# Performance work log

Measured on AMD Instinct MI355X. Metric: run time of the kernel, lower is better.

The kernel has to match this reference:

```python
import jax, jax.numpy as jnp
import numpy as np

T = 8            # num edge basis features (static)
E = 8388608      # num edges
N = 262144       # num output nodes
F = 64           # filters


def setup_inputs() -> dict:
    key = jax.random.key(0)
    k1, k2, k3 = jax.random.split(key, 3)
    edge_features = jax.random.normal(k1, (T, E), dtype=jnp.float32)
    sparse_indices = jax.random.randint(k2, (E, 2), 0, N, dtype=jnp.int64)
    kernel = jax.random.normal(k3, (T, F), dtype=jnp.float32) * 0.1
    bias = jnp.zeros((F,), dtype=jnp.float32)
    return {
        "edge_features": edge_features,
        "sparse_indices": sparse_indices,
        "out_size": N,
        "kernel": kernel,
        "bias": bias,
    }


def reference(edge_features, sparse_indices, out_size, kernel, bias):
    # edge_features: [T, E]; sparse_indices: [E, 2] (row = output node id)
    rows = sparse_indices[:, 0]
    # Aggregate per-edge features into nodes: [N, T]
    agg = jax.ops.segment_sum(edge_features.T, rows, num_segments=out_size)
    # Dense projection + bias (activation is None / linear)
    out = agg @ kernel + bias  # [N, F]
    return out
```

## Files before the change

kernel.cpp:

```cpp
#include <hip/hip_runtime.h>
#include <hip/hip_fp16.h>

typedef unsigned int uint;

#define T_DIM 8
#define F_DIM 64
#define BUCKETS 256
#define RPB 1024
#define RPB_SHIFT 10
#define CAP 36864
#define SC_BLOCKS 1024
#define SC_THREADS 512
#define SUB 2048
#define EPT (SUB / SC_THREADS)
#define NSUB 4
#define ACH 3072

__device__ __forceinline__ uint pack_h2(float a, float b) {
  union { __half2 h2; uint u32; } cvt;
  cvt.h2 = __floats2half2_rn(a, b);
  return cvt.u32;
}
__device__ __forceinline__ float2 unpack_h2(uint v) {
  union { uint u32; __half2 h2; } cvt;
  cvt.u32 = v;
  return __half22float2(cvt.h2);
}


__global__ __launch_bounds__(SC_THREADS) void scatter_sort_kernel(
    const uint* __restrict__ idx, const float* __restrict__ ef,
    uint* __restrict__ cursor, unsigned short* __restrict__ rows_out,
    uint4* __restrict__ recs_out, int E) {
  __shared__ uint hist[BUCKETS];
  __shared__ uint lbase[BUCKETS];
  __shared__ uint gdelta[BUCKETS];
  __shared__ uint wpart4[4];
  __shared__ uint wpre4[4];
  __shared__ uint srows[SUB];
  __shared__ uint4 srecs[SUB];
  __shared__ int s_is64;
  const int tid = threadIdx.x;
  const int lane = tid & 63;
  const int wid = tid >> 6;
  if (tid == 0) {
    uint acc = 0;
    for (int i = 1; i < 64; i += 2) acc |= idx[i];
    s_is64 = (acc == 0);
  }
  __syncthreads();
  const bool is64 = (s_is64 != 0);
  const int cstart = blockIdx.x * (SUB * NSUB);

  for (int sc = 0; sc < NSUB; ++sc) {
    const int base = cstart + sc * SUB;
    if (tid < BUCKETS) hist[tid] = 0;
    __syncthreads();

    uint r[EPT];
#pragma unroll
    for (int j = 0; j < EPT; ++j) {
      const uint e = base + j * SC_THREADS + tid;
      r[j] = is64 ? idx[(size_t)e << 2] : idx[(size_t)e << 1];
      atomicAdd(&hist[r[j] >> RPB_SHIFT], 1u);
    }
    __syncthreads();

    uint cntb = 0, x = 0;
    if (tid < BUCKETS) {
      cntb = hist[tid];
      x = cntb;
    }
    for (int o = 1; o < 64; o <<= 1) {
      const uint y = __shfl_up(x, o, 64);
      if (lane >= o) x += y;
    }
    if (tid < BUCKETS && lane == 63) wpart4[wid] = x;
    __syncthreads();
    if (tid == 0) {
      uint run = 0;
#pragma unroll
      for (int w = 0; w < 4; ++w) {
        const uint t = wpart4[w];
        wpre4[w] = run;
        run += t;
      }
    }
    __syncthreads();
    if (tid < BUCKETS) {
      const uint excl = wpre4[wid] + x - cntb;
      lbase[tid] = excl;
      const uint gb = atomicAdd(&cursor[tid], cntb);
      gdelta[tid] = (uint)tid * CAP + gb - excl;
      hist[tid] = 0;
    }
    __syncthreads();

#pragma unroll
    for (int j = 0; j < EPT; ++j) {
      const uint e = base + j * SC_THREADS + tid;
      const uint row = r[j];
      const uint bkt = row >> RPB_SHIFT;
      const uint p = lbase[bkt] + atomicAdd(&hist[bkt], 1u);
      float v[T_DIM];
#pragma unroll
      for (int t = 0; t < T_DIM; ++t) v[t] = ef[(size_t)t * E + e];
      uint4 rec;
      rec.x = pack_h2(v[0], v[1]);
      rec.y = pack_h2(v[2], v[3]);
      rec.z = pack_h2(v[4], v[5]);
      rec.w = pack_h2(v[6], v[7]);
      srows[p] = row;
      srecs[p] = rec;
    }
    __syncthreads();

#pragma unroll
    for (int j = 0; j < EPT; ++j) {
      const uint i = j * SC_THREADS + tid;
      const uint row = srows[i];
      const uint dst = gdelta[row >> RPB_SHIFT] + i;
      rows_out[dst] = (unsigned short)(row & (RPB - 1));
      recs_out[dst] = srecs[i];
    }
    __syncthreads();
  }
}

__global__ __launch_bounds__(1024) void accum_mm_kernel(
    const unsigned short* __restrict__ rows, const uint4* __restrict__ recs,
    const uint* __restrict__ cursor, const float* __restrict__ kern,
    const float* __restrict__ bias, float* __restrict__ out) {
  __shared__ uint4 sRec[ACH];
  __shared__ uint hist[RPB];
  __shared__ uint wpart[16];
  __shared__ float sK[T_DIM * F_DIM];
  __shared__ float sB[F_DIM];
  const int tid = threadIdx.x;
  const int lane = tid & 63;
  const int wid = tid >> 6;
  const int b = blockIdx.x;
  if (tid < T_DIM * F_DIM / 4) ((float4*)sK)[tid] = ((const float4*)kern)[tid];
  if (tid < F_DIM / 4) ((float4*)sB)[tid] = ((const float4*)bias)[tid];
  const uint cnt = cursor[b];
  const size_t rbase = (size_t)b * CAP;
  float acc[T_DIM];
#pragma unroll
  for (int t = 0; t < T_DIM; ++t) acc[t] = 0.f;

  for (uint c0 = 0; c0 < cnt; c0 += ACH) {
    const uint m = (cnt - c0 < ACH) ? (cnt - c0) : ACH;
    hist[tid] = 0;
    __syncthreads();

    uint rloc[ACH / 1024];
    uint4 rv[ACH / 1024];
#pragma unroll
    for (int j = 0; j < ACH / 1024; ++j) {
      const uint i = (uint)(j * 1024) + tid;
      if (i < m) {
        rloc[j] = rows[rbase + c0 + i];
        rv[j] = recs[rbase + c0 + i];
        atomicAdd(&hist[rloc[j]], 1u);
      }
    }
    __syncthreads();

    const uint mycnt = hist[tid];
    uint x = mycnt;
    for (int o = 1; o < 64; o <<= 1) {
      const uint y = __shfl_up(x, o, 64);
      if (lane >= o) x += y;
    }
    if (lane == 63) wpart[wid] = x;
    __syncthreads();
    if (wid == 0) {
      uint p = (lane < 16) ? wpart[lane] : 0;
      for (int o = 1; o < 16; o <<= 1) {
        const uint y = __shfl_up(p, o, 64);
        if (lane >= o) p += y;
      }
      if (lane < 16) wpart[lane] = p;
    }
    __syncthreads();
    const uint wbase = (wid == 0) ? 0u : wpart[wid - 1];
    const uint mystart = wbase + x - mycnt;
    hist[tid] = mystart;
    __syncthreads();

#pragma unroll
    for (int j = 0; j < ACH / 1024; ++j) {
      const uint i = (uint)(j * 1024) + tid;
      if (i < m) {
        const uint p = atomicAdd(&hist[rloc[j]], 1u);
        sRec[p] = rv[j];
      }
    }
    __syncthreads();

    for (uint k = 0; k < mycnt; ++k) {
      const uint4 v = sRec[mystart + k];
      const float2 f0 = unpack_h2(v.x);
      const float2 f1 = unpack_h2(v.y);
      const float2 f2 = unpack_h2(v.z);
      const float2 f3 = unpack_h2(v.w);
      acc[0] += f0.x; acc[1] += f0.y;
      acc[2] += f1.x; acc[3] += f1.y;
      acc[4] += f2.x; acc[5] += f2.y;
      acc[6] += f3.x; acc[7] += f3.y;
    }
    __syncthreads();
  }

  float* sAgg = (float*)sRec;
#pragma unroll
  for (int t = 0; t < T_DIM; ++t) sAgg[tid * 9 + t] = acc[t];
  __syncthreads();

  const uint base_row = (uint)b << RPB_SHIFT;
  for (int w = tid; w < RPB * 16; w += 1024) {
    const int rr = w >> 4, q = w & 15;
    const float* a = &sAgg[rr * 9];
    float4 o4 = ((const float4*)sB)[q];
#pragma unroll
    for (int t = 0; t < T_DIM; ++t) {
      const float4 kv = ((const float4*)sK)[t * 16 + q];
      const float av = a[t];
      o4.x += av * kv.x;
      o4.y += av * kv.y;
      o4.z += av * kv.z;
      o4.w += av * kv.w;
    }
    *(float4*)(out + (size_t)(base_row + rr) * F_DIM + (q << 2)) = o4;
  }
}


__global__ __launch_bounds__(256) void scatter_agg_kernel(
    const uint* __restrict__ idx, const float* __restrict__ ef,
    float* __restrict__ agg, int E) {
  __shared__ int s_is64;
  if (threadIdx.x == 0) {
    uint acc = 0;
    for (int i = 1; i < 64; i += 2) acc |= idx[i];
    s_is64 = (acc == 0) ? 1 : 0;
  }
  __syncthreads();
  const bool is64 = (s_is64 != 0);
  const long long base = ((long long)blockIdx.x * blockDim.x + threadIdx.x) * 4;
  if (base >= E) return;
  int rows[4];
  if (is64) {
#pragma unroll
    for (int j = 0; j < 4; ++j) rows[j] = (int)idx[(size_t)(base + j) << 2];
  } else {
#pragma unroll
    for (int j = 0; j < 4; ++j) rows[j] = (int)idx[(size_t)(base + j) << 1];
  }
  float4 v[T_DIM];
#pragma unroll
  for (int t = 0; t < T_DIM; ++t)
    v[t] = *(const float4*)(ef + (size_t)t * E + base);
#pragma unroll
  for (int j = 0; j < 4; ++j) {
    float* dst = agg + (size_t)rows[j] * T_DIM;
#pragma unroll
    for (int t = 0; t < T_DIM; ++t)
      unsafeAtomicAdd(dst + t, ((const float*)&v[t])[j]);
  }
}

__global__ __launch_bounds__(256) void mm_kernel(
    const float* __restrict__ agg, const float* __restrict__ kern,
    const float* __restrict__ bias, float* __restrict__ out, int N) {
  __shared__ float sK[T_DIM * F_DIM];
  __shared__ float sB[F_DIM];
  const int tid = threadIdx.x;
  if (tid < (T_DIM * F_DIM / 4)) ((float4*)sK)[tid] = ((const float4*)kern)[tid];
  if (tid < F_DIM / 4) ((float4*)sB)[tid] = ((const float4*)bias)[tid];
  __syncthreads();
  const long long gid = (long long)blockIdx.x * blockDim.x + tid;
  const int n = (int)(gid >> 4);
  if (n >= N) return;
  const int q = (int)(gid & 15);
  const float4 a0 = *(const float4*)(agg + (size_t)n * T_DIM);
  const float4 a1 = *(const float4*)(agg + (size_t)n * T_DIM + 4);
  const float a[T_DIM] = {a0.x, a0.y, a0.z, a0.w, a1.x, a1.y, a1.z, a1.w};
  float4 r = ((const float4*)sB)[q];
#pragma unroll
  for (int t = 0; t < T_DIM; ++t) {
    const float4 kv = ((const float4*)sK)[t * (F_DIM / 4) + q];
    r.x += a[t] * kv.x;
    r.y += a[t] * kv.y;
    r.z += a[t] * kv.z;
    r.w += a[t] * kv.w;
  }
  *(float4*)(out + (size_t)n * F_DIM + (q << 2)) = r;
}

extern "C" void kernel_launch(void* const* d_in, const int* in_sizes, int n_in,
                              void* d_out, int out_size, void* d_ws,
                              size_t ws_size, hipStream_t stream) {
  const float* ef = (const float*)d_in[0];
  const uint* idx = (const uint*)d_in[1];
  const float* kern = (const float*)d_in[3];
  const float* bias = (const float*)d_in[4];
  float* out = (float*)d_out;

  const int E = in_sizes[1] / 2;
  const int N = out_size / F_DIM;

  size_t off = 0;
  auto carve = [&](size_t bytes) {
    void* p = (char*)d_ws + off;
    off += (bytes + 255) & ~(size_t)255;
    return p;
  };
  uint4* recs = (uint4*)carve((size_t)BUCKETS * CAP * sizeof(uint4));
  unsigned short* rows =
      (unsigned short*)carve((size_t)BUCKETS * CAP * sizeof(unsigned short));
  uint* cursor = (uint*)carve(BUCKETS * sizeof(uint));

  const bool fast = (E == SC_BLOCKS * SUB * NSUB) && (N == BUCKETS * RPB) &&
                    (off <= ws_size);
  if (fast) {
    hipMemsetAsync(cursor, 0, BUCKETS * sizeof(uint), stream);
    scatter_sort_kernel<<<SC_BLOCKS, SC_THREADS, 0, stream>>>(
        idx, ef, cursor, rows, recs, E);
    accum_mm_kernel<<<BUCKETS, 1024, 0, stream>>>(rows, recs, cursor, kern,
                                                  bias, out);
  } else {
    float* agg = (float*)d_ws;
    hipMemsetAsync(agg, 0, (size_t)N * T_DIM * sizeof(float), stream);
    scatter_agg_kernel<<<(E / 4 + 255) / 256, 256, 0, stream>>>(idx, ef, agg,
                                                                E);
    mm_kernel<<<(int)(((long long)N * 16 + 255) / 256), 256, 0, stream>>>(
        agg, kern, bias, out, N);
  }
}
```

Before: 587.6 us.

## Use 512 row buckets and prefetch next chunk in accumulate kernel

Doubles the bucket count to 512 (512 rows each), so the accumulate kernel launches 512 blocks of 512 threads instead of 256 blocks of 1024, giving more blocks to spread across CUs. The accumulate loop now issues global loads for the next chunk into registers while the current chunk is counting-sorted and summed, hiding load latency behind the shared-memory work. In exchange, the scatter kernel does more cursor atomics and more scattered writes per sub-chunk, and register pressure rises from the double-buffered records.

```diff
diff --git a/kernel.cpp b/kernel.cpp
--- a/kernel.cpp
+++ b/kernel.cpp
@@ -5,16 +5,18 @@
 
 #define T_DIM 8
 #define F_DIM 64
-#define BUCKETS 256
-#define RPB 1024
-#define RPB_SHIFT 10
-#define CAP 36864
+#define BUCKETS 512
+#define RPB 512
+#define RPB_SHIFT 9
+#define CAP 18432
 #define SC_BLOCKS 1024
 #define SC_THREADS 512
 #define SUB 2048
 #define EPT (SUB / SC_THREADS)
 #define NSUB 4
-#define ACH 3072
+#define ACH 2048
+#define AC_THREADS 512
+#define AEPT (ACH / AC_THREADS)
 
 __device__ __forceinline__ uint pack_h2(float a, float b) {
   union { __half2 h2; uint u32; } cvt;
@@ -35,8 +37,8 @@
   __shared__ uint hist[BUCKETS];
   __shared__ uint lbase[BUCKETS];
   __shared__ uint gdelta[BUCKETS];
-  __shared__ uint wpart4[4];
-  __shared__ uint wpre4[4];
+  __shared__ uint wpart[8];
+  __shared__ uint wpre[8];
   __shared__ uint srows[SUB];
   __shared__ uint4 srecs[SUB];
   __shared__ int s_is64;
@@ -54,7 +56,7 @@
 
   for (int sc = 0; sc < NSUB; ++sc) {
     const int base = cstart + sc * SUB;
-    if (tid < BUCKETS) hist[tid] = 0;
+    hist[tid] = 0;
     __syncthreads();
 
     uint r[EPT];
@@ -66,34 +68,29 @@
     }
     __syncthreads();
 
-    uint cntb = 0, x = 0;
-    if (tid < BUCKETS) {
-      cntb = hist[tid];
-      x = cntb;
-    }
+    const uint cntb = hist[tid];
+    uint x = cntb;
     for (int o = 1; o < 64; o <<= 1) {
       const uint y = __shfl_up(x, o, 64);
       if (lane >= o) x += y;
     }
-    if (tid < BUCKETS && lane == 63) wpart4[wid] = x;
+    if (lane == 63) wpart[wid] = x;
     __syncthreads();
     if (tid == 0) {
       uint run = 0;
 #pragma unroll
-      for (int w = 0; w < 4; ++w) {
-        const uint t = wpart4[w];
-        wpre4[w] = run;
+      for (int w = 0; w < 8; ++w) {
+        const uint t = wpart[w];
+        wpre[w] = run;
         run += t;
       }
     }
     __syncthreads();
-    if (tid < BUCKETS) {
-      const uint excl = wpre4[wid] + x - cntb;
-      lbase[tid] = excl;
-      const uint gb = atomicAdd(&cursor[tid], cntb);
-      gdelta[tid] = (uint)tid * CAP + gb - excl;
-      hist[tid] = 0;
-    }
+    const uint excl = wpre[wid] + x - cntb;
+    lbase[tid] = excl;
+    const uint gb = atomicAdd(&cursor[tid], cntb);
+    gdelta[tid] = (uint)tid * CAP + gb - excl;
+    hist[tid] = 0;
     __syncthreads();
 
 #pragma unroll
@@ -127,13 +124,14 @@
   }
 }
 
-__global__ __launch_bounds__(1024) void accum_mm_kernel(
+__global__ __launch_bounds__(AC_THREADS) void accum_mm_kernel(
     const unsigned short* __restrict__ rows, const uint4* __restrict__ recs,
     const uint* __restrict__ cursor, const float* __restrict__ kern,
     const float* __restrict__ bias, float* __restrict__ out) {
   __shared__ uint4 sRec[ACH];
   __shared__ uint hist[RPB];
-  __shared__ uint wpart[16];
+  __shared__ uint wpart[8];
+  __shared__ uint wpre[8];
   __shared__ float sK[T_DIM * F_DIM];
   __shared__ float sB[F_DIM];
   const int tid = threadIdx.x;
@@ -148,21 +146,33 @@
 #pragma unroll
   for (int t = 0; t < T_DIM; ++t) acc[t] = 0.f;
 
+  uint nloc[AEPT];
+  uint4 nv[AEPT];
+  {
+    const uint m0 = (cnt < ACH) ? cnt : ACH;
+#pragma unroll
+    for (int j = 0; j < AEPT; ++j) {
+      const uint i = (uint)(j * AC_THREADS) + tid;
+      if (i < m0) {
+        nloc[j] = rows[rbase + i];
+        nv[j] = recs[rbase + i];
+      }
+    }
+  }
+
   for (uint c0 = 0; c0 < cnt; c0 += ACH) {
     const uint m = (cnt - c0 < ACH) ? (cnt - c0) : ACH;
+    uint rloc[AEPT];
+    uint4 rv[AEPT];
+#pragma unroll
+    for (int j = 0; j < AEPT; ++j) { rloc[j] = nloc[j]; rv[j] = nv[j]; }
     hist[tid] = 0;
     __syncthreads();
 
-    uint rloc[ACH / 1024];
-    uint4 rv[ACH / 1024];
-#pragma unroll
-    for (int j = 0; j < ACH / 1024; ++j) {
-      const uint i = (uint)(j * 1024) + tid;
-      if (i < m) {
-        rloc[j] = rows[rbase + c0 + i];
-        rv[j] = recs[rbase + c0 + i];
-        atomicAdd(&hist[rloc[j]], 1u);
-      }
+#pragma unroll
+    for (int j = 0; j < AEPT; ++j) {
+      const uint i = (uint)(j * AC_THREADS) + tid;
+      if (i < m) atomicAdd(&hist[rloc[j]], 1u);
     }
     __syncthreads();
 
@@ -174,26 +184,38 @@
     }
     if (lane == 63) wpart[wid] = x;
     __syncthreads();
-    if (wid == 0) {
-      uint p = (lane < 16) ? wpart[lane] : 0;
-      for (int o = 1; o < 16; o <<= 1) {
-        const uint y = __shfl_up(p, o, 64);
-        if (lane >= o) p += y;
-      }
-      if (lane < 16) wpart[lane] = p;
-    }
-    __syncthreads();
-    const uint wbase = (wid == 0) ? 0u : wpart[wid - 1];
-    const uint mystart = wbase + x - mycnt;
+    if (tid == 0) {
+      uint run = 0;
+#pragma unroll
+      for (int w = 0; w < 8; ++w) {
+        const uint t = wpart[w];
+        wpre[w] = run;
+        run += t;
+      }
+    }
+    __syncthreads();
+    const uint mystart = wpre[wid] + x - mycnt;
     hist[tid] = mystart;
     __syncthreads();
 
 #pragma unroll
-    for (int j = 0; j < ACH / 1024; ++j) {
-      const uint i = (uint)(j * 1024) + tid;
+    for (int j = 0; j < AEPT; ++j) {
+      const uint i = (uint)(j * AC_THREADS) + tid;
       if (i < m) {
         const uint p = atomicAdd(&hist[rloc[j]], 1u);
         sRec[p] = rv[j];
+      }
+    }
+    const uint c1 = c0 + ACH;
+    if (c1 < cnt) {
+      const uint m1 = (cnt - c1 < ACH) ? (cnt - c1) : ACH;
+#pragma unroll
+      for (int j = 0; j < AEPT; ++j) {
+        const uint i = (uint)(j * AC_THREADS) + tid;
+        if (i < m1) {
+          nloc[j] = rows[rbase + c1 + i];
+          nv[j] = recs[rbase + c1 + i];
+        }
       }
     }
     __syncthreads();
@@ -218,7 +240,7 @@
   __syncthreads();
 
   const uint base_row = (uint)b << RPB_SHIFT;
-  for (int w = tid; w < RPB * 16; w += 1024) {
+  for (int w = tid; w < RPB * 16; w += AC_THREADS) {
     const int rr = w >> 4, q = w & 15;
     const float* a = &sAgg[rr * 9];
     float4 o4 = ((const float4*)sB)[q];
@@ -327,8 +349,8 @@
     hipMemsetAsync(cursor, 0, BUCKETS * sizeof(uint), stream);
     scatter_sort_kernel<<<SC_BLOCKS, SC_THREADS, 0, stream>>>(
         idx, ef, cursor, rows, recs, E);
-    accum_mm_kernel<<<BUCKETS, 1024, 0, stream>>>(rows, recs, cursor, kern,
-                                                  bias, out);
+    accum_mm_kernel<<<BUCKETS, AC_THREADS, 0, stream>>>(rows, recs, cursor,
+                                                        kern, bias, out);
   } else {
     float* agg = (float*)d_ws;
     hipMemsetAsync(agg, 0, (size_t)N * T_DIM * sizeof(float), stream);
```

New measurement: 657.4 us. 11.9% more time.
